# Kernel optimization log

Measured on AMD Instinct MI355X. Metric: run time of the kernel, lower is better.

The kernel has to match this reference:

```python
import jax, jax.numpy as jnp
import numpy as np

N, E = 50000, 800000
NODE_IN, HID, EMB, HEADS = 64, 64, 32, 4


def setup_inputs() -> dict:
    key = jax.random.key(0)
    ks = jax.random.split(key, 12)
    s = 0.1
    return {
        "x": jax.random.normal(ks[0], (N, NODE_IN), jnp.float32),
        "edge_index": jax.random.randint(ks[1], (2, E), 0, N, jnp.int32),
        "edge_weight": jax.random.uniform(ks[2], (E,), jnp.float32),
        # GCNConv: lin weight [out,in], bias [out]
        "W1": jax.random.normal(ks[3], (HID, NODE_IN), jnp.float32) * s,
        "b1": jnp.zeros((HID,), jnp.float32),
        # GATv2Conv: lin_l/lin_r [H*C, in] with bias, lin_edge [H*C, 1] no bias,
        # att [H, C], output bias [C] (concat=False)
        "Wl": jax.random.normal(ks[4], (HEADS * EMB, HID), jnp.float32) * s,
        "bl": jnp.zeros((HEADS * EMB,), jnp.float32),
        "Wr": jax.random.normal(ks[5], (HEADS * EMB, HID), jnp.float32) * s,
        "br": jnp.zeros((HEADS * EMB,), jnp.float32),
        "We": jax.random.normal(ks[6], (HEADS * EMB, 1), jnp.float32) * s,
        "att": jax.random.normal(ks[7], (HEADS, EMB), jnp.float32) * s,
        "bias_gat": jnp.zeros((EMB,), jnp.float32),
        # residual skip Linear(node_in_dim -> emb_dim) and gate
        "Ws": jax.random.normal(ks[8], (EMB, NODE_IN), jnp.float32) * s,
        "bs": jnp.zeros((EMB,), jnp.float32),
        "skip_gate": jnp.float32(1.0),
    }


def _gcn(x, src, dst, w, W1, b1):
    # PyG GCNConv with edge_weight: add self-loops (weight 1), sym norm D^-1/2 A D^-1/2
    loop = jnp.arange(N, dtype=src.dtype)
    src2 = jnp.concatenate([src, loop])
    dst2 = jnp.concatenate([dst, loop])
    w2 = jnp.concatenate([w, jnp.ones((N,), w.dtype)])
    deg = jax.ops.segment_sum(w2, dst2, num_segments=N)
    dinv = jnp.where(deg > 0, jax.lax.rsqrt(jnp.maximum(deg, 1e-30)), 0.0)
    norm = dinv[src2] * w2 * dinv[dst2]  # [E2]
    h = x @ W1.T  # [N, HID]
    return jax.ops.segment_sum(h[src2] * norm[:, None], dst2, num_segments=N) + b1


def _gatv2(h, src, dst, edge_attr, Wl, bl, Wr, br, We, att, bias_gat):
    # self-loops with edge_attr fill_value='mean' (mean of incoming edge_attr per node)
    loop = jnp.arange(N, dtype=src.dtype)
    la_sum = jax.ops.segment_sum(edge_attr, dst, num_segments=N)  # [N,1]
    cnt = jax.ops.segment_sum(jnp.ones_like(edge_attr), dst, num_segments=N)
    loop_attr = jnp.where(cnt > 0, la_sum / jnp.maximum(cnt, 1.0), 0.0)
    src2 = jnp.concatenate([src, loop])
    dst2 = jnp.concatenate([dst, loop])
    ea = jnp.concatenate([edge_attr, loop_attr], axis=0)  # [E2, 1]
    xl = (h @ Wl.T + bl).reshape(N, HEADS, EMB)  # source transform
    xr = (h @ Wr.T + br).reshape(N, HEADS, EMB)  # target transform
    ee = (ea @ We.T).reshape(-1, HEADS, EMB)     # edge transform
    m = jax.nn.leaky_relu(xl[src2] + xr[dst2] + ee, 0.2)  # [E2,H,C]
    alpha = jnp.einsum('ehc,hc->eh', m, att)  # [E2,H]
    amax = jax.ops.segment_max(alpha, dst2, num_segments=N)
    ex = jnp.exp(alpha - amax[dst2])
    denom = jax.ops.segment_sum(ex, dst2, num_segments=N)
    a = ex / (denom[dst2] + 1e-16)  # edge softmax per target node
    out = jax.ops.segment_sum(xl[src2] * a[:, :, None], dst2, num_segments=N)
    return out.mean(axis=1) + bias_gat  # concat=False -> head mean


def reference(x, edge_index, edge_weight, W1, b1, Wl, bl, Wr, br, We, att,
              bias_gat, Ws, bs, skip_gate):
    src, dst = edge_index[0], edge_index[1]
    h = jax.nn.relu(_gcn(x, src, dst, edge_weight, W1, b1))
    # dropout is identity in eval mode
    z = _gatv2(h, src, dst, edge_weight[:, None], Wl, bl, Wr, br, We, att, bias_gat)
    return z + skip_gate * (x @ Ws.T + bs)
```

## Files before the change

### kernel.cpp

```cpp
#include <hip/hip_runtime.h>
#include <hip/hip_bf16.h>

typedef unsigned int uint;
typedef unsigned short ushort;
typedef unsigned long long ull;
typedef __attribute__((ext_vector_type(8))) short short8v;
typedef __attribute__((ext_vector_type(4))) float f32x4;

#define PAD 96

__device__ __forceinline__ float bflo(uint u) { return __uint_as_float(u << 16); }
__device__ __forceinline__ float bfhi(uint u) { return __uint_as_float(u & 0xffff0000u); }
__device__ __forceinline__ float bfu(ushort s) { return __uint_as_float(((uint)s) << 16); }
__device__ __forceinline__ ushort f2bf(float f) {
    uint u = __float_as_uint(f);
    u += 0x7fffu + ((u >> 16) & 1u);
    return (ushort)(u >> 16);
}
__device__ __forceinline__ uint pk2(float lo, float hi) {
    return (uint)f2bf(lo) | ((uint)f2bf(hi) << 16);
}
__device__ __forceinline__ float red4(float v) {
    v += __shfl_xor(v, 1, 64);
    v += __shfl_xor(v, 2, 64);
    return v;
}
__device__ __forceinline__ float lrelu(float v) { return (v > 0.f) ? v : 0.2f * v; }
__device__ __forceinline__ void unp8(uint4 u, float* f) {
    f[0] = bflo(u.x); f[1] = bfhi(u.x);
    f[2] = bflo(u.y); f[3] = bfhi(u.y);
    f[4] = bflo(u.z); f[5] = bfhi(u.z);
    f[6] = bflo(u.w); f[7] = bfhi(u.w);
}

__global__ __launch_bounds__(256) void k_init(ull* pk, int n,
                                              const float* __restrict__ W1,
                                              const float* __restrict__ Wl,
                                              const float* __restrict__ Wr,
                                              ushort* w1b, ushort* wlb, ushort* wrb) {
    int i = blockIdx.x * blockDim.x + threadIdx.x;
    if (i < n) pk[i] = 0ULL;
    if (i < 4096) w1b[i] = f2bf(W1[i]);
    if (i < 8192) { wlb[i] = f2bf(Wl[i]); wrb[i] = f2bf(Wr[i]); }
}

__global__ __launch_bounds__(256) void k_rank_gx(const int* __restrict__ src,
                                                 const int* __restrict__ dst,
                                                 const float* __restrict__ w,
                                                 ull* pk, int2* eSW, int E,
                                                 int rnkBlocks,
                                                 const float* __restrict__ X,
                                                 const ushort* __restrict__ W1b,
                                                 ushort* __restrict__ hb, int Mt) {
    if (blockIdx.x < rnkBlocks) {
        int e = blockIdx.x * blockDim.x + threadIdx.x;
        if (e < E) {
            int d = dst[e];
            float we = w[e];
            ull add = (1ULL << 40) | (ull)(uint)(we * 16777216.0f);
            ull old = atomicAdd(&pk[d], add);
            uint r = (uint)(old >> 40);
            if (r < PAD)
                eSW[(size_t)d * PAD + r] = make_int2(src[e], __float_as_int(we));
        }
        return;
    }
    const int wv = (blockIdx.x - rnkBlocks) * 4 + (threadIdx.x >> 6);
    if (wv >= Mt) return;
    const int lane = threadIdx.x & 63;
    const int r16 = lane & 15, kseg = lane >> 4;
    const float* xr = X + ((size_t)(wv * 16 + r16)) * 64 + kseg * 8;
    float4 x0 = *(const float4*)xr;
    float4 x1 = *(const float4*)(xr + 4);
    float4 x2 = *(const float4*)(xr + 32);
    float4 x3 = *(const float4*)(xr + 36);
    short8v a0, a1;
    a0[0] = (short)f2bf(x0.x); a0[1] = (short)f2bf(x0.y);
    a0[2] = (short)f2bf(x0.z); a0[3] = (short)f2bf(x0.w);
    a0[4] = (short)f2bf(x1.x); a0[5] = (short)f2bf(x1.y);
    a0[6] = (short)f2bf(x1.z); a0[7] = (short)f2bf(x1.w);
    a1[0] = (short)f2bf(x2.x); a1[1] = (short)f2bf(x2.y);
    a1[2] = (short)f2bf(x2.z); a1[3] = (short)f2bf(x2.w);
    a1[4] = (short)f2bf(x3.x); a1[5] = (short)f2bf(x3.y);
    a1[6] = (short)f2bf(x3.z); a1[7] = (short)f2bf(x3.w);
    const short8v* Wv = (const short8v*)W1b;
    f32x4 acc[4];
#pragma unroll
    for (int t = 0; t < 4; t++) acc[t] = (f32x4){0.f, 0.f, 0.f, 0.f};
#pragma unroll
    for (int t = 0; t < 4; t++) {
        int col = t * 16 + r16;
        acc[t] = __builtin_amdgcn_mfma_f32_16x16x32_bf16(a0, Wv[col * 8 + kseg], acc[t], 0, 0, 0);
        acc[t] = __builtin_amdgcn_mfma_f32_16x16x32_bf16(a1, Wv[col * 8 + 4 + kseg], acc[t], 0, 0, 0);
    }
#pragma unroll
    for (int t = 0; t < 4; t++)
#pragma unroll
        for (int i = 0; i < 4; i++)
            hb[((size_t)(wv * 16 + kseg * 4 + i)) * 64 + t * 16 + r16] = f2bf(acc[t][i]);
}

__global__ __launch_bounds__(256) void k_nodeprep(const ull* __restrict__ pk,
                                                  int* __restrict__ cnt,
                                                  float* __restrict__ dinv,
                                                  float* __restrict__ lattr, int n) {
    int i = blockIdx.x * blockDim.x + threadIdx.x;
    if (i < n) {
        ull pv = pk[i];
        int c = (int)(pv >> 40);
        float sw = (float)(pv & 0xFFFFFFFFFFULL) * 5.9604644775390625e-8f;
        cnt[i] = c;
        dinv[i] = rsqrtf(sw + 1.f);
        lattr[i] = (c > 0) ? sw / (float)c : 0.f;
    }
}

__global__ __launch_bounds__(256) void k_gemm_lr(const ushort* __restrict__ Ab,
                                                 const ushort* __restrict__ WLb,
                                                 const float* __restrict__ BL,
                                                 const ushort* __restrict__ WRb,
                                                 const float* __restrict__ BR,
                                                 ushort* __restrict__ YL,
                                                 ushort* __restrict__ YR, int Mt) {
    const int wv = blockIdx.x * 4 + (threadIdx.x >> 6);
    if (wv >= Mt) return;
    const int lane = threadIdx.x & 63;
    const int r16 = lane & 15, kseg = lane >> 4;
    const short8v* arow = (const short8v*)(Ab + ((size_t)(wv * 16 + r16)) * 64);
    short8v a0 = arow[kseg], a1 = arow[4 + kseg];
    const short8v* WvL = (const short8v*)WLb;
    const short8v* WvR = (const short8v*)WRb;
    f32x4 accL[8], accR[8];
#pragma unroll
    for (int t = 0; t < 8; t++) {
        accL[t] = (f32x4){0.f, 0.f, 0.f, 0.f};
        accR[t] = (f32x4){0.f, 0.f, 0.f, 0.f};
    }
#pragma unroll
    for (int t = 0; t < 8; t++) {
        int col = t * 16 + r16;
        accL[t] = __builtin_amdgcn_mfma_f32_16x16x32_bf16(a0, WvL[col * 8 + kseg], accL[t], 0, 0, 0);
        accL[t] = __builtin_amdgcn_mfma_f32_16x16x32_bf16(a1, WvL[col * 8 + 4 + kseg], accL[t], 0, 0, 0);
        accR[t] = __builtin_amdgcn_mfma_f32_16x16x32_bf16(a0, WvR[col * 8 + kseg], accR[t], 0, 0, 0);
        accR[t] = __builtin_amdgcn_mfma_f32_16x16x32_bf16(a1, WvR[col * 8 + 4 + kseg], accR[t], 0, 0, 0);
    }
#pragma unroll
    for (int t = 0; t < 8; t++) {
        int col = t * 16 + r16;
        float blv = BL[col], brv = BR[col];
#pragma unroll
        for (int i = 0; i < 4; i++) {
            size_t row = (size_t)(wv * 16 + kseg * 4 + i);
            YL[row * 128 + col] = f2bf(accL[t][i] + blv);
            YR[row * 128 + col] = f2bf(accR[t][i] + brv);
        }
    }
}

__global__ __launch_bounds__(256) void k_gcn_agg(const ushort* __restrict__ hb,
                                                 const int* __restrict__ cnt,
                                                 const int2* __restrict__ eSW,
                                                 const float* __restrict__ dinv,
                                                 const float* __restrict__ b1,
                                                 ushort* __restrict__ hgb, int nN) {
    const int lane = threadIdx.x & 63;
    const int gwid = blockIdx.x * 4 + (threadIdx.x >> 6);
    const int nwv = gridDim.x * 4;
    const int g = lane >> 3, sub = lane & 7;
    const char* hB = (const char*)hb;
    const uint so = (uint)sub * 16u;

    for (int node = gwid; node < nN; node += nwv) {
        const float di = dinv[node];
        float acc[8] = {0.f, 0.f, 0.f, 0.f, 0.f, 0.f, 0.f, 0.f};
        const int beg = node * PAD, endr = beg + cnt[node];
        int e0 = beg + g, e1 = e0 + 8;
        bool v0 = e0 < endr, v1 = e1 < endr;
        int2 q0 = v0 ? eSW[e0] : make_int2(node, 0);
        int2 q1 = v1 ? eSW[e1] : make_int2(node, 0);
        for (int base = beg; base < endr; base += 16) {
            uint4 u0 = *(const uint4*)(hB + (((uint)q0.x) << 7) + so);
            uint4 u1 = *(const uint4*)(hB + (((uint)q1.x) << 7) + so);
            float n0 = v0 ? dinv[q0.x] * __int_as_float(q0.y) * di : 0.f;
            float n1 = v1 ? dinv[q1.x] * __int_as_float(q1.y) * di : 0.f;
            int nb = base + 16;
            e0 = nb + g; e1 = e0 + 8;
            v0 = e0 < endr; v1 = e1 < endr;
            q0 = v0 ? eSW[e0] : make_int2(node, 0);
            q1 = v1 ? eSW[e1] : make_int2(node, 0);
            float xa[8], xb[8];
            unp8(u0, xa); unp8(u1, xb);
#pragma unroll
            for (int j = 0; j < 8; j++)
                acc[j] = fmaf(n0, xa[j], fmaf(n1, xb[j], acc[j]));
        }
#pragma unroll
        for (int j = 0; j < 8; j++) {
            acc[j] += __shfl_xor(acc[j], 8, 64);
            acc[j] += __shfl_xor(acc[j], 16, 64);
            acc[j] += __shfl_xor(acc[j], 32, 64);
        }
        if (g == 0) {
            const int c0 = sub * 8;
            uint4 hv = *(const uint4*)(hB + (((uint)node) << 7) + so);
            float h8[8];
            unp8(hv, h8);
            float4 ba = *(const float4*)(b1 + c0);
            float4 bb = *(const float4*)(b1 + c0 + 4);
            float di2 = di * di;
            float o[8];
            o[0] = fmaxf(fmaf(di2, h8[0], acc[0]) + ba.x, 0.f);
            o[1] = fmaxf(fmaf(di2, h8[1], acc[1]) + ba.y, 0.f);
            o[2] = fmaxf(fmaf(di2, h8[2], acc[2]) + ba.z, 0.f);
            o[3] = fmaxf(fmaf(di2, h8[3], acc[3]) + ba.w, 0.f);
            o[4] = fmaxf(fmaf(di2, h8[4], acc[4]) + bb.x, 0.f);
            o[5] = fmaxf(fmaf(di2, h8[5], acc[5]) + bb.y, 0.f);
            o[6] = fmaxf(fmaf(di2, h8[6], acc[6]) + bb.z, 0.f);
            o[7] = fmaxf(fmaf(di2, h8[7], acc[7]) + bb.w, 0.f);
            uint4 ov;
            ov.x = pk2(o[0], o[1]);
            ov.y = pk2(o[2], o[3]);
            ov.z = pk2(o[4], o[5]);
            ov.w = pk2(o[6], o[7]);
            *(uint4*)((char*)hgb + (((uint)node) << 7) + so) = ov;
        }
    }
}

__global__ __launch_bounds__(256) void k_gat_fused(const uint* __restrict__ XL,
                                                   const uint* __restrict__ XR,
                                                   const int* __restrict__ cnt,
                                                   const int2* __restrict__ eSW,
                                                   const float* __restrict__ lattr,
                                                   const float* __restrict__ We,
                                                   const float* __restrict__ att,
                                                   const float* __restrict__ bias_gat,
                                                   const float* __restrict__ x,
                                                   const float* __restrict__ Ws,
                                                   const float* __restrict__ bs,
                                                   const float* __restrict__ sgp,
                                                   float* __restrict__ out, int nN) {
    __shared__ float lds[4 * 608];
    const int lane = threadIdx.x & 63;
    const int wv = threadIdx.x >> 6;
    float* L = lds + wv * 608;
    const int g = lane >> 4, sub = lane & 15;
    const int hh = sub >> 2;
    const int c0 = sub * 8;
    const int gwid = blockIdx.x * 4 + wv;
    const int nwv = gridDim.x * 4;

    float We8[8], att8[8];
#pragma unroll
    for (int j = 0; j < 8; j++) { We8[j] = We[c0 + j]; att8[j] = att[c0 + j]; }
    const int cs = lane & 31, h0 = lane >> 5;
    const float bgv = bias_gat[cs], bsv = bs[cs], sgv = sgp[0];
    const char* XLb = (const char*)XL;
    const ushort* XLus = (const ushort*)XL;
    const uint so = (uint)sub * 16u;

    for (int node = gwid; node < nN; node += nwv) {
        uint4 ur = *(const uint4*)((const char*)XR + (((uint)node) << 8) + so);
        float xr8[8];
        unp8(ur, xr8);

        float acc[8] = {0.f, 0.f, 0.f, 0.f, 0.f, 0.f, 0.f, 0.f};
        float den = 0.f;
        const int beg = node * PAD, endr = beg + cnt[node];
        int e0 = beg + g, e1 = e0 + 4;
        bool v0 = e0 < endr, v1 = e1 < endr;
        int2 q0 = v0 ? eSW[e0] : make_int2(node, 0);
        int2 q1 = v1 ? eSW[e1] : make_int2(node, 0);
        for (int base = beg; base < endr; base += 8) {
            uint4 u0 = *(const uint4*)(XLb + (((uint)q0.x) << 8) + so);
            uint4 u1 = *(const uint4*)(XLb + (((uint)q1.x) << 8) + so);
            float w0 = __int_as_float(q0.y), w1 = __int_as_float(q1.y);
            bool cv0 = v0, cv1 = v1;
            int nb = base + 8;
            e0 = nb + g; e1 = e0 + 4;
            v0 = e0 < endr; v1 = e1 < endr;
            q0 = v0 ? eSW[e0] : make_int2(node, 0);
            q1 = v1 ? eSW[e1] : make_int2(node, 0);
            float xa[8], xb[8];
            unp8(u0, xa); unp8(u1, xb);
            float t0 = 0.f, t1 = 0.f;
#pragma unroll
            for (int j = 0; j < 8; j++) {
                float s = xr8[j], aj = att8[j], wj = We8[j];
                t0 = fmaf(lrelu(fmaf(w0, wj, xa[j] + s)), aj, t0);
                t1 = fmaf(lrelu(fmaf(w1, wj, xb[j] + s)), aj, t1);
            }
            t0 = red4(t0);
            t1 = red4(t1);
            float ex0 = cv0 ? __expf(t0) : 0.f;
            float ex1 = cv1 ? __expf(t1) : 0.f;
            den += ex0 + ex1;
#pragma unroll
            for (int j = 0; j < 8; j++)
                acc[j] = fmaf(ex0, xa[j], fmaf(ex1, xb[j], acc[j]));
        }

        float la = lattr[node];
        uint4 un = *(const uint4*)(XLb + (((uint)node) << 8) + so);
        float xn[8];
        unp8(un, xn);
        float ts = 0.f;
#pragma unroll
        for (int j = 0; j < 8; j++)
            ts = fmaf(lrelu(fmaf(la, We8[j], xn[j] + xr8[j])), att8[j], ts);
        ts = red4(ts);
        float es = __expf(ts);

#pragma unroll
        for (int j = 0; j < 8; j++) L[lane * 9 + j] = acc[j];
        if ((sub & 3) == 0) L[576 + g * 4 + hh] = den;
        if (g == 0 && (sub & 3) == 0) L[592 + hh] = es;

        float th = 0.f;
#pragma unroll
        for (int hd = 0; hd < 4; hd++) {
            int bl = hd * 4 + (cs >> 3);
            int j = cs & 7;
            float a = L[bl * 9 + j] + L[(16 + bl) * 9 + j] +
                      L[(32 + bl) * 9 + j] + L[(48 + bl) * 9 + j];
            float dn = L[576 + hd] + L[580 + hd] + L[584 + hd] + L[588 + hd];
            float eh = L[592 + hd];
            float xc = bfu(XLus[(size_t)node * 128 + hd * 32 + cs]);
            th += (a + eh * xc) / (dn + eh + 1e-16f);
        }
        const float4* xp = (const float4*)(x + (size_t)node * 64 + h0 * 32);
        const float4* wp = (const float4*)(Ws + (size_t)cs * 64 + h0 * 32);
        float sk = 0.f;
#pragma unroll
        for (int q = 0; q < 8; q++) {
            float4 xq = xp[q], wq = wp[q];
            sk += xq.x * wq.x + xq.y * wq.y + xq.z * wq.z + xq.w * wq.w;
        }
        sk += __shfl_xor(sk, 32, 64);
        float res = th * 0.25f + bgv + sgv * (sk + bsv);
        if (lane < 32) out[(size_t)node * 32 + cs] = res;
    }
}

extern "C" void kernel_launch(void* const* d_in, const int* in_sizes, int n_in,
                              void* d_out, int out_size, void* d_ws, size_t ws_size,
                              hipStream_t stream) {
    const float* x        = (const float*)d_in[0];
    const int*   ei       = (const int*)d_in[1];
    const float* ew       = (const float*)d_in[2];
    const float* W1       = (const float*)d_in[3];
    const float* b1       = (const float*)d_in[4];
    const float* Wl       = (const float*)d_in[5];
    const float* bl       = (const float*)d_in[6];
    const float* Wr       = (const float*)d_in[7];
    const float* br       = (const float*)d_in[8];
    const float* We       = (const float*)d_in[9];
    const float* att      = (const float*)d_in[10];
    const float* bias_gat = (const float*)d_in[11];
    const float* Ws       = (const float*)d_in[12];
    const float* bs       = (const float*)d_in[13];
    const float* sg       = (const float*)d_in[14];

    const int N = in_sizes[0] / 64;
    const int E = in_sizes[2];
    const int* srcI = ei;
    const int* dstI = ei + E;
    const int nblk = (N + 255) / 256;
    const int Mt = (N + 15) / 16;
    const int rnkBlocks = (E + 255) / 256;
    const int gxBlocks = (Mt + 3) / 4;
    const int initBlocks = ((N > 8192 ? N : 8192) + 255) / 256;

    char* p = (char*)d_ws;
    auto alloc = [&](size_t bytes) {
        void* r = (void*)p;
        p += (bytes + 255) & ~(size_t)255;
        return r;
    };
    ull*    pk     = (ull*)alloc((size_t)N * 8);
    int*    cnt    = (int*)alloc((size_t)N * 4);
    int2*   eSW    = (int2*)alloc((size_t)N * PAD * 8);
    float*  dinv   = (float*)alloc((size_t)N * 4);
    float*  lattr  = (float*)alloc((size_t)N * 4);
    ushort* hb     = (ushort*)alloc((size_t)Mt * 16 * 64 * 2);
    ushort* hgb    = (ushort*)alloc((size_t)Mt * 16 * 64 * 2);
    ushort* xl_bf  = (ushort*)alloc((size_t)Mt * 16 * 128 * 2);
    ushort* xr_bf  = (ushort*)alloc((size_t)Mt * 16 * 128 * 2);
    ushort* w1b    = (ushort*)alloc(4096 * 2);
    ushort* wlb    = (ushort*)alloc(8192 * 2);
    ushort* wrb    = (ushort*)alloc(8192 * 2);
    if ((size_t)(p - (char*)d_ws) > ws_size) return;

    k_init<<<initBlocks, 256, 0, stream>>>(pk, N, W1, Wl, Wr, w1b, wlb, wrb);
    k_rank_gx<<<rnkBlocks + gxBlocks, 256, 0, stream>>>(srcI, dstI, ew, pk, eSW, E,
                                                        rnkBlocks, x, w1b, hb, Mt);
    k_nodeprep<<<nblk, 256, 0, stream>>>(pk, cnt, dinv, lattr, N);
    k_gcn_agg<<<2048, 256, 0, stream>>>(hb, cnt, eSW, dinv, b1, hgb, N);
    k_gemm_lr<<<(Mt + 3) / 4, 256, 0, stream>>>(hgb, wlb, bl, wrb, br,
                                                xl_bf, xr_bf, Mt);
    k_gat_fused<<<2048, 256, 0, stream>>>((const uint*)xl_bf, (const uint*)xr_bf,
                                          cnt, eSW, lattr, We, att,
                                          bias_gat, x, Ws, bs, sg,
                                          (float*)d_out, N);
}
```

Baseline: 189.0 us.

## Store GATv2 source/target features in FP8 and rewrite leaky-relu via abs

The GEMM now writes the per-node XL/XR feature tables as FP8 instead of bf16, which halves the bytes gathered per edge in the fused GAT aggregation. The attention score's leaky-relu is rewritten as 0.6*v + 0.4*|v|, so the per-element select becomes two FMA accumulations. The risk is accuracy: FP8 has roughly 3 mantissa bits, and the quantization error flows into both the attention logits and the aggregated output values.

```diff
diff --git a/kernel.cpp b/kernel.cpp
--- a/kernel.cpp
+++ b/kernel.cpp
@@ -3,15 +3,16 @@
 
 typedef unsigned int uint;
 typedef unsigned short ushort;
+typedef unsigned char uchar;
 typedef unsigned long long ull;
 typedef __attribute__((ext_vector_type(8))) short short8v;
 typedef __attribute__((ext_vector_type(4))) float f32x4;
+typedef __attribute__((ext_vector_type(2))) float f32x2;
 
 #define PAD 96
 
 __device__ __forceinline__ float bflo(uint u) { return __uint_as_float(u << 16); }
 __device__ __forceinline__ float bfhi(uint u) { return __uint_as_float(u & 0xffff0000u); }
-__device__ __forceinline__ float bfu(ushort s) { return __uint_as_float(((uint)s) << 16); }
 __device__ __forceinline__ ushort f2bf(float f) {
     uint u = __float_as_uint(f);
     u += 0x7fffu + ((u >> 16) & 1u);
@@ -20,17 +21,27 @@
 __device__ __forceinline__ uint pk2(float lo, float hi) {
     return (uint)f2bf(lo) | ((uint)f2bf(hi) << 16);
 }
+__device__ __forceinline__ uchar f2fp8(float v) {
+    return (uchar)(__builtin_amdgcn_cvt_pk_fp8_f32(v, v, 0, false) & 0xff);
+}
 __device__ __forceinline__ float red4(float v) {
     v += __shfl_xor(v, 1, 64);
     v += __shfl_xor(v, 2, 64);
     return v;
 }
-__device__ __forceinline__ float lrelu(float v) { return (v > 0.f) ? v : 0.2f * v; }
 __device__ __forceinline__ void unp8(uint4 u, float* f) {
     f[0] = bflo(u.x); f[1] = bfhi(u.x);
     f[2] = bflo(u.y); f[3] = bfhi(u.y);
     f[4] = bflo(u.z); f[5] = bfhi(u.z);
     f[6] = bflo(u.w); f[7] = bfhi(u.w);
+}
+__device__ __forceinline__ void unpf8(uint2 u, float* f) {
+    f32x2 p0 = __builtin_amdgcn_cvt_pk_f32_fp8(u.x, false);
+    f32x2 p1 = __builtin_amdgcn_cvt_pk_f32_fp8(u.x, true);
+    f32x2 p2 = __builtin_amdgcn_cvt_pk_f32_fp8(u.y, false);
+    f32x2 p3 = __builtin_amdgcn_cvt_pk_f32_fp8(u.y, true);
+    f[0] = p0.x; f[1] = p0.y; f[2] = p1.x; f[3] = p1.y;
+    f[4] = p2.x; f[5] = p2.y; f[6] = p3.x; f[7] = p3.y;
 }
 
 __global__ __launch_bounds__(256) void k_init(ull* pk, int n,
@@ -120,8 +131,8 @@
                                                  const float* __restrict__ BL,
                                                  const ushort* __restrict__ WRb,
                                                  const float* __restrict__ BR,
-                                                 ushort* __restrict__ YL,
-                                                 ushort* __restrict__ YR, int Mt) {
+                                                 uchar* __restrict__ YL,
+                                                 uchar* __restrict__ YR, int Mt) {
     const int wv = blockIdx.x * 4 + (threadIdx.x >> 6);
     if (wv >= Mt) return;
     const int lane = threadIdx.x & 63;
@@ -151,8 +162,8 @@
 #pragma unroll
         for (int i = 0; i < 4; i++) {
             size_t row = (size_t)(wv * 16 + kseg * 4 + i);
-            YL[row * 128 + col] = f2bf(accL[t][i] + blv);
-            YR[row * 128 + col] = f2bf(accR[t][i] + brv);
+            YL[row * 128 + col] = f2fp8(accL[t][i] + blv);
+            YR[row * 128 + col] = f2fp8(accR[t][i] + brv);
         }
     }
 }
@@ -227,8 +238,8 @@
     }
 }
 
-__global__ __launch_bounds__(256) void k_gat_fused(const uint* __restrict__ XL,
-                                                   const uint* __restrict__ XR,
+__global__ __launch_bounds__(256) void k_gat_fused(const uchar* __restrict__ XL,
+                                                   const uchar* __restrict__ XR,
                                                    const int* __restrict__ cnt,
                                                    const int2* __restrict__ eSW,
                                                    const float* __restrict__ lattr,
@@ -255,14 +266,12 @@
     for (int j = 0; j < 8; j++) { We8[j] = We[c0 + j]; att8[j] = att[c0 + j]; }
     const int cs = lane & 31, h0 = lane >> 5;
     const float bgv = bias_gat[cs], bsv = bs[cs], sgv = sgp[0];
-    const char* XLb = (const char*)XL;
-    const ushort* XLus = (const ushort*)XL;
-    const uint so = (uint)sub * 16u;
+    const uint so8 = (uint)sub * 8u;
 
     for (int node = gwid; node < nN; node += nwv) {
-        uint4 ur = *(const uint4*)((const char*)XR + (((uint)node) << 8) + so);
+        uint2 ur = *(const uint2*)(XR + (((uint)node) << 7) + so8);
         float xr8[8];
-        unp8(ur, xr8);
+        unpf8(ur, xr8);
 
         float acc[8] = {0.f, 0.f, 0.f, 0.f, 0.f, 0.f, 0.f, 0.f};
         float den = 0.f;
@@ -272,8 +281,8 @@
         int2 q0 = v0 ? eSW[e0] : make_int2(node, 0);
         int2 q1 = v1 ? eSW[e1] : make_int2(node, 0);
         for (int base = beg; base < endr; base += 8) {
-            uint4 u0 = *(const uint4*)(XLb + (((uint)q0.x) << 8) + so);
-            uint4 u1 = *(const uint4*)(XLb + (((uint)q1.x) << 8) + so);
+            uint2 u0 = *(const uint2*)(XL + (((uint)q0.x) << 7) + so8);
+            uint2 u1 = *(const uint2*)(XL + (((uint)q1.x) << 7) + so8);
             float w0 = __int_as_float(q0.y), w1 = __int_as_float(q1.y);
             bool cv0 = v0, cv1 = v1;
             int nb = base + 8;
@@ -282,16 +291,20 @@
             q0 = v0 ? eSW[e0] : make_int2(node, 0);
             q1 = v1 ? eSW[e1] : make_int2(node, 0);
             float xa[8], xb[8];
-            unp8(u0, xa); unp8(u1, xb);
-            float t0 = 0.f, t1 = 0.f;
+            unpf8(u0, xa); unpf8(u1, xb);
+            float tl0 = 0.f, ta0 = 0.f, tl1 = 0.f, ta1 = 0.f;
 #pragma unroll
             for (int j = 0; j < 8; j++) {
-                float s = xr8[j], aj = att8[j], wj = We8[j];
-                t0 = fmaf(lrelu(fmaf(w0, wj, xa[j] + s)), aj, t0);
-                t1 = fmaf(lrelu(fmaf(w1, wj, xb[j] + s)), aj, t1);
+                float aj = att8[j], wj = We8[j], rj = xr8[j];
+                float va = xa[j] + fmaf(w0, wj, rj);
+                float vb = xb[j] + fmaf(w1, wj, rj);
+                tl0 = fmaf(va, aj, tl0);
+                ta0 = fmaf(fabsf(va), aj, ta0);
+                tl1 = fmaf(vb, aj, tl1);
+                ta1 = fmaf(fabsf(vb), aj, ta1);
             }
-            t0 = red4(t0);
-            t1 = red4(t1);
+            float t0 = red4(fmaf(0.4f, ta0, 0.6f * tl0));
+            float t1 = red4(fmaf(0.4f, ta1, 0.6f * tl1));
             float ex0 = cv0 ? __expf(t0) : 0.f;
             float ex1 = cv1 ? __expf(t1) : 0.f;
             den += ex0 + ex1;
@@ -301,14 +314,17 @@
         }
 
         float la = lattr[node];
-        uint4 un = *(const uint4*)(XLb + (((uint)node) << 8) + so);
+        uint2 un = *(const uint2*)(XL + (((uint)node) << 7) + so8);
         float xn[8];
-        unp8(un, xn);
-        float ts = 0.f;
-#pragma unroll
-        for (int j = 0; j < 8; j++)
-            ts = fmaf(lrelu(fmaf(la, We8[j], xn[j] + xr8[j])), att8[j], ts);
-        ts = red4(ts);
+        unpf8(un, xn);
+        float tls = 0.f, tas = 0.f;
+#pragma unroll
+        for (int j = 0; j < 8; j++) {
+            float v = xn[j] + fmaf(la, We8[j], xr8[j]);
+            tls = fmaf(v, att8[j], tls);
+            tas = fmaf(fabsf(v), att8[j], tas);
+        }
+        float ts = red4(fmaf(0.4f, tas, 0.6f * tls));
         float es = __expf(ts);
 
 #pragma unroll
@@ -325,7 +341,9 @@
                       L[(32 + bl) * 9 + j] + L[(48 + bl) * 9 + j];
             float dn = L[576 + hd] + L[580 + hd] + L[584 + hd] + L[588 + hd];
             float eh = L[592 + hd];
-            float xc = bfu(XLus[(size_t)node * 128 + hd * 32 + cs]);
+            uint wrd = *(const uint*)(XL + (((size_t)node) << 7) + hd * 32 + (cs & ~3));
+            uint b0 = (wrd >> ((cs & 3) * 8)) & 0xffu;
+            float xc = __builtin_amdgcn_cvt_f32_fp8(b0, 0);
             th += (a + eh * xc) / (dn + eh + 1e-16f);
         }
         const float4* xp = (const float4*)(x + (size_t)node * 64 + h0 * 32);
@@ -384,8 +402,8 @@
     float*  lattr  = (float*)alloc((size_t)N * 4);
     ushort* hb     = (ushort*)alloc((size_t)Mt * 16 * 64 * 2);
     ushort* hgb    = (ushort*)alloc((size_t)Mt * 16 * 64 * 2);
-    ushort* xl_bf  = (ushort*)alloc((size_t)Mt * 16 * 128 * 2);
-    ushort* xr_bf  = (ushort*)alloc((size_t)Mt * 16 * 128 * 2);
+    uchar*  xl_f8  = (uchar*)alloc((size_t)Mt * 16 * 128);
+    uchar*  xr_f8  = (uchar*)alloc((size_t)Mt * 16 * 128);
     ushort* w1b    = (ushort*)alloc(4096 * 2);
     ushort* wlb    = (ushort*)alloc(8192 * 2);
     ushort* wrb    = (ushort*)alloc(8192 * 2);
@@ -397,9 +415,8 @@
     k_nodeprep<<<nblk, 256, 0, stream>>>(pk, cnt, dinv, lattr, N);
     k_gcn_agg<<<2048, 256, 0, stream>>>(hb, cnt, eSW, dinv, b1, hgb, N);
     k_gemm_lr<<<(Mt + 3) / 4, 256, 0, stream>>>(hgb, wlb, bl, wrb, br,
-                                                xl_bf, xr_bf, Mt);
-    k_gat_fused<<<2048, 256, 0, stream>>>((const uint*)xl_bf, (const uint*)xr_bf,
-                                          cnt, eSW, lattr, We, att,
+                                                xl_f8, xr_f8, Mt);
+    k_gat_fused<<<2048, 256, 0, stream>>>(xl_f8, xr_f8, cnt, eSW, lattr, We, att,
                                           bias_gat, x, Ws, bs, sg,
                                           (float*)d_out, N);
 }
```

New measurement: 184.5 us. -2.4%, faster.
